# Optimization experiments

Measured on AMD Instinct MI355X. Metric: run time of the kernel, lower is better.

The kernel has to match this reference:

```python
import jax, jax.numpy as jnp
import numpy as np

H, KVH, D = 32, 8, 64  # n_heads, n_kv_heads, head_dim
NREP = H // KVH


def _rope(x, cos, sin):
    # x: (B,T,h,D); cos/sin: (T, D//2)
    half = x.shape[-1] // 2
    x1, x2 = x[..., :half], x[..., half:]
    c = cos[None, :, None, :]
    s = sin[None, :, None, :]
    return jnp.concatenate([x1 * c - x2 * s, x1 * s + x2 * c], axis=-1).astype(x.dtype)


def setup_inputs() -> dict:
    key = jax.random.key(0)
    k1, k2, k3 = jax.random.split(key, 3)
    B, T, C = 1, 2048, 2048
    x = jax.random.normal(k1, (B, T, C), dtype=jnp.float32)
    # real RoPE tables (base 10000), shape (T, D//2)
    inv_freq = 1.0 / (10000.0 ** (np.arange(0, D, 2, dtype=np.float32) / D))
    t = np.arange(T, dtype=np.float32)
    freqs = np.outer(t, inv_freq)
    cos = jnp.asarray(np.cos(freqs))
    sin = jnp.asarray(np.sin(freqs))
    Wqkv = jax.random.normal(k2, (C, H * D + 2 * KVH * D), dtype=jnp.float32) * (C ** -0.5)
    Wo = jax.random.normal(k3, (H * D, C), dtype=jnp.float32) * ((H * D) ** -0.5)
    return {"x": x, "cos": cos, "sin": sin, "Wqkv": Wqkv, "Wo": Wo}


def reference(x, cos, sin, Wqkv, Wo):
    B, T, C = x.shape
    qkv = x @ Wqkv  # (B,T, H*D + 2*KVH*D)
    q = qkv[..., : H * D].reshape(B, T, H, D)
    k = qkv[..., H * D : H * D + KVH * D].reshape(B, T, KVH, D)
    v = qkv[..., H * D + KVH * D :].reshape(B, T, KVH, D)
    # cast to bf16 as in the torch module
    q, k, v = q.astype(jnp.bfloat16), k.astype(jnp.bfloat16), v.astype(jnp.bfloat16)
    q = _rope(q, cos, sin)
    k = _rope(k, cos, sin)
    # GQA without materializing repeated KV: split q heads into (kv_head, rep)
    qg = q.reshape(B, T, KVH, NREP, D)
    scale = jnp.asarray(1.0 / np.sqrt(D), dtype=jnp.bfloat16)
    scores = jnp.einsum("bqhrd,bkhd->bhrqk", qg, k) * scale  # (B,KVH,NREP,T,T) bf16
    causal = jnp.tril(jnp.ones((T, T), dtype=bool))
    scores = jnp.where(causal[None, None, None], scores, jnp.asarray(-jnp.inf, scores.dtype))
    attn = jax.nn.softmax(scores.astype(jnp.float32), axis=-1).astype(q.dtype)
    out = jnp.einsum("bhrqk,bkhd->bqhrd", attn, v).reshape(B, T, H * D)
    return out.astype(jnp.float32) @ Wo
```

## Files before the change

### kernel.cpp

```cpp
#include <hip/hip_runtime.h>
#include <hip/hip_bf16.h>
#include <cstdint>
#include <cstddef>

#define T_SEQ 2048
#define C_DIM 2048
#define NQKV  3072
#define HQ    32
#define KVH_  8
#define D_HEAD 64

using bf16x8 = __attribute__((ext_vector_type(8))) __bf16;
using f32x4  = __attribute__((ext_vector_type(4))) float;

typedef const __attribute__((address_space(1))) void* gas_ptr;
typedef __attribute__((address_space(3))) void* las_ptr;
#define GLOAD_LDS16(g, l) __builtin_amdgcn_global_load_lds((gas_ptr)(g), (las_ptr)(l), 16, 0, 0)

static __device__ __forceinline__ unsigned short f2bf(float f) {
  union { float f; unsigned int u; } v; v.f = f;
  unsigned int u = v.u;
  unsigned int r = u + 0x7fffu + ((u >> 16) & 1u);
  return (unsigned short)(r >> 16);
}
static __device__ __forceinline__ float bf2f(unsigned short s) {
  union { unsigned int u; float f; } v; v.u = ((unsigned int)s) << 16;
  return v.f;
}
static __device__ __forceinline__ bf16x8 load8(const unsigned short* p) {
  return *reinterpret_cast<const bf16x8*>(p);
}
static __device__ __forceinline__ f32x4 mfma16(bf16x8 a, bf16x8 b, f32x4 c) {
  return __builtin_amdgcn_mfma_f32_16x16x32_bf16(a, b, c, 0, 0, 0);
}

static __device__ const unsigned char kF2QG[40] = {
    15, 15, 15, 15, 14, 14, 14, 13, 13, 13, 12, 12, 12, 11, 11,
    10, 10, 9, 9, 8, 8, 7, 7, 6, 5, 4, 3,
    14, 11, 6, 2, 13, 10, 5, 1, 12, 9, 8, 4, 0};
static __device__ const unsigned char kF2SEG[40] = {
    0, 1, 2, 3, 0, 1, 2, 0, 1, 2, 0, 1, 2, 0, 1,
    0, 1, 0, 1, 0, 1, 0, 1, 0, 0, 0, 0,
    3, 2, 1, 0, 3, 2, 1, 0, 3, 2, 2, 1, 0};
static __device__ const unsigned char kQGF[16][4] = {
    {39, 0, 0, 0}, {34, 0, 0, 0}, {30, 0, 0, 0}, {26, 0, 0, 0},
    {25, 38, 0, 0}, {24, 33, 0, 0}, {23, 29, 0, 0}, {21, 22, 0, 0},
    {19, 20, 37, 0}, {17, 18, 36, 0}, {15, 16, 32, 0}, {13, 14, 28, 0},
    {10, 11, 12, 35}, {7, 8, 9, 31}, {4, 5, 6, 27}, {0, 1, 2, 3}};

__global__ __launch_bounds__(256) void cast_x_kernel(
    const float* __restrict__ x, unsigned short* __restrict__ xh) {
  const int i = (blockIdx.x * 256 + threadIdx.x) * 8;
  const float4 a = *reinterpret_cast<const float4*>(x + i);
  const float4 b = *reinterpret_cast<const float4*>(x + i + 4);
  ushort h[8];
  h[0] = f2bf(a.x); h[1] = f2bf(a.y); h[2] = f2bf(a.z); h[3] = f2bf(a.w);
  h[4] = f2bf(b.x); h[5] = f2bf(b.y); h[6] = f2bf(b.z); h[7] = f2bf(b.w);
  *reinterpret_cast<uint4*>(xh + i) = *reinterpret_cast<const uint4*>(h);
}

__global__ __launch_bounds__(256) void transpose_cast_kernel(
    const float* __restrict__ src, unsigned short* __restrict__ dhi, int R, int C) {
  __shared__ float tile[64][65];
  const int r0 = blockIdx.y * 64, c0 = blockIdx.x * 64;
  const int tid = threadIdx.x;
  const int lr = tid >> 4, lc = (tid & 15) * 4;
  for (int i = 0; i < 4; ++i) {
    const int row = lr + i * 16;
    const float4 v = *reinterpret_cast<const float4*>(&src[(size_t)(r0 + row) * C + c0 + lc]);
    tile[row][lc + 0] = v.x; tile[row][lc + 1] = v.y;
    tile[row][lc + 2] = v.z; tile[row][lc + 3] = v.w;
  }
  __syncthreads();
  for (int i = 0; i < 4; ++i) {
    const int n = lr + i * 16;
    ushort4 h;
    h.x = f2bf(tile[lc + 0][n]); h.y = f2bf(tile[lc + 1][n]);
    h.z = f2bf(tile[lc + 2][n]); h.w = f2bf(tile[lc + 3][n]);
    *reinterpret_cast<ushort4*>(&dhi[(size_t)(c0 + n) * R + r0 + lc]) = h;
  }
}

__global__ __launch_bounds__(256, 2) void gemm1_kernel(
    const unsigned short* __restrict__ Xh, const unsigned short* __restrict__ BTh,
    const float* __restrict__ cosb, const float* __restrict__ sinb,
    unsigned short* __restrict__ qkv) {
  __shared__ unsigned short Ah[64 * 64], Bh[128 * 64];
  const int tid = threadIdx.x;
  const int orig = (int)blockIdx.y * 24 + (int)blockIdx.x;
  const int wgid = (orig & 7) * 96 + (orig >> 3);
  const int n0 = (wgid % 24) * 128, m0 = (wgid / 24) * 64;
  const int lane = tid & 63, wave = tid >> 6;
  const int wm = wave >> 1, wn = wave & 1;
  const int lrow = lane & 15, g = lane >> 4;
  const int srow8 = lane >> 3, pchunk = lane & 7;
  const int swz = lrow & 7;
  f32x4 acc[2][4] = {};
  for (int kb = 0; kb < C_DIM; kb += 64) {
    __syncthreads();
    for (int p = 0; p < 2; ++p) {
      const int row = (p * 4 + wave) * 8 + srow8;
      const int gcol = (pchunk ^ srow8) * 8;
      GLOAD_LDS16(&Xh[(size_t)(m0 + row) * C_DIM + kb + gcol],
                  &Ah[row * 64 + pchunk * 8]);
    }
    for (int p = 0; p < 4; ++p) {
      const int row = (p * 4 + wave) * 8 + srow8;
      const int gcol = (pchunk ^ srow8) * 8;
      GLOAD_LDS16(&BTh[(size_t)(n0 + row) * C_DIM + kb + gcol],
                  &Bh[row * 64 + pchunk * 8]);
    }
    __syncthreads();
    for (int kk = 0; kk < 2; ++kk) {
      bf16x8 ah[2], bh[4];
      const int cc = ((kk * 4 + g) ^ swz) * 8;
      for (int i = 0; i < 2; ++i)
        ah[i] = load8(&Ah[(wm * 32 + i * 16 + lrow) * 64 + cc]);
      for (int i = 0; i < 4; ++i)
        bh[i] = load8(&Bh[(wn * 64 + i * 16 + lrow) * 64 + cc]);
      for (int mi = 0; mi < 2; ++mi)
        for (int ni = 0; ni < 4; ++ni)
          acc[mi][ni] = mfma16(ah[mi], bh[ni], acc[mi][ni]);
    }
  }
  const int colbase = n0 + wn * 64;
  const bool isv = colbase >= (C_DIM + KVH_ * D_HEAD);
  const float qsc = (colbase < C_DIM) ? 0.18033688011112042f : 1.0f;
  for (int mi = 0; mi < 2; ++mi) {
    for (int r = 0; r < 4; ++r) {
      const int trow = m0 + wm * 32 + mi * 16 + g * 4 + r;
      if (!isv) {
        for (int ni = 0; ni < 2; ++ni) {
          const int dh = ni * 16 + lrow;
          const float c = cosb[trow * 32 + dh];
          const float s = sinb[trow * 32 + dh];
          const float a = bf2f(f2bf(acc[mi][ni][r]));
          const float b = bf2f(f2bf(acc[mi][ni + 2][r]));
          qkv[(size_t)trow * NQKV + colbase + dh]      = f2bf((a * c - b * s) * qsc);
          qkv[(size_t)trow * NQKV + colbase + dh + 32] = f2bf((a * s + b * c) * qsc);
        }
      } else {
        for (int ni = 0; ni < 4; ++ni)
          qkv[(size_t)trow * NQKV + colbase + ni * 16 + lrow] = f2bf(acc[mi][ni][r]);
      }
    }
  }
}

__global__ __launch_bounds__(256) void vt_kernel(const unsigned short* __restrict__ qkv,
                                                 unsigned short* __restrict__ vt) {
  __shared__ unsigned short tile[64][72];
  const int t0 = blockIdx.x * 64, j0 = blockIdx.y * 64;
  const int tid = threadIdx.x;
  const int lr = tid >> 4, lc = (tid & 15) * 4;
  for (int i = 0; i < 4; ++i) {
    const int row = lr + i * 16;
    const ushort4 v = *reinterpret_cast<const ushort4*>(
        &qkv[(size_t)(t0 + row) * NQKV + (C_DIM + KVH_ * D_HEAD) + j0 + lc]);
    *reinterpret_cast<ushort4*>(&tile[row][lc]) = v;
  }
  __syncthreads();
  for (int i = 0; i < 4; ++i) {
    const int j = lr + i * 16;
    ushort4 v;
    v.x = tile[lc + 0][j]; v.y = tile[lc + 1][j];
    v.z = tile[lc + 2][j]; v.w = tile[lc + 3][j];
    *reinterpret_cast<ushort4*>(&vt[(size_t)(j0 + j) * T_SEQ + t0 + lc]) = v;
  }
}

__global__ __launch_bounds__(256, 3) void attn_seg_kernel(
    const unsigned short* __restrict__ qkv, const unsigned short* __restrict__ Vt,
    unsigned short* __restrict__ po, float2* __restrict__ pml) {
  __shared__ unsigned short kbuf[2][64 * 64];
  __shared__ unsigned short vbuf[2][64 * 64];
  __shared__ unsigned short plds[4][2][16][72];
  const int f = blockIdx.x, h = blockIdx.y;
  const int qg = kF2QG[f];
  const int seg = kF2SEG[f];
  const int slot = h * 40 + f;
  const int tid = threadIdx.x;
  const int wave = tid >> 6, lane = tid & 63;
  const int kvh = h >> 2;
  const int q0b = qg * 128;
  const int q0 = q0b + wave * 32;
  const int lrow = lane & 15, g = lane >> 4;

  const int t0 = seg * 8;
  const int t1 = min(t0 + 8, 2 * qg + 2);

  const int srow = lane >> 3;
  const int schunk = (lane & 7) ^ srow;
  const unsigned short* Kg = qkv + C_DIM + kvh * D_HEAD;

  bf16x8 qf[2][2];
  for (int qs = 0; qs < 2; ++qs)
    for (int dc = 0; dc < 2; ++dc)
      qf[qs][dc] = load8(&qkv[(size_t)(q0 + qs * 16 + lrow) * NQKV + h * D_HEAD + dc * 32 + g * 8]);

  f32x4 o[2][4] = {};
  float l_[2] = {0.f, 0.f};
  const int swz = (lrow & 7);

  {
    const int k00 = t0 * 64;
    for (int j = 0; j < 2; ++j) {
      const int r0 = wave * 16 + j * 8;
      GLOAD_LDS16(Kg + (size_t)(k00 + r0 + srow) * NQKV + schunk * 8,
                  &kbuf[0][r0 * 64 + lane * 8]);
      GLOAD_LDS16(Vt + (size_t)(kvh * 64 + r0 + srow) * T_SEQ + k00 + schunk * 8,
                  &vbuf[0][r0 * 64 + lane * 8]);
    }
  }
  __syncthreads();

  for (int t = t0; t < t1; ++t) {
    const int cur = (t - t0) & 1;
    const int k0 = t * 64;
    if (t + 1 < t1) {
      const int k0n = k0 + 64;
      for (int j = 0; j < 2; ++j) {
        const int r0 = wave * 16 + j * 8;
        GLOAD_LDS16(Kg + (size_t)(k0n + r0 + srow) * NQKV + schunk * 8,
                    &kbuf[cur ^ 1][r0 * 64 + lane * 8]);
        GLOAD_LDS16(Vt + (size_t)(kvh * 64 + r0 + srow) * T_SEQ + k0n + schunk * 8,
                    &vbuf[cur ^ 1][r0 * 64 + lane * 8]);
      }
    }

    if (k0 <= q0 + 31) {
      const bool maskt = (k0 + 63 > q0);

      f32x4 s[4][2] = {};
      __builtin_amdgcn_s_setprio(1);
      for (int kt = 0; kt < 4; ++kt) {
        const unsigned short* krow = &kbuf[cur][(kt * 16 + lrow) * 64];
        const bf16x8 kf0 = load8(krow + ((0 * 4 + g) ^ swz) * 8);
        const bf16x8 kf1 = load8(krow + ((1 * 4 + g) ^ swz) * 8);
        for (int qs = 0; qs < 2; ++qs) {
          s[kt][qs] = mfma16(kf0, qf[qs][0], s[kt][qs]);
          s[kt][qs] = mfma16(kf1, qf[qs][1], s[kt][qs]);
        }
      }
      __builtin_amdgcn_s_setprio(0);

      for (int qs = 0; qs < 2; ++qs) {
        float rs = 0.f;
        for (int kt = 0; kt < 4; ++kt)
          for (int r = 0; r < 4; ++r) {
            float v = (float)(__bf16)(s[kt][qs][r]);
            if (maskt) {
              const int ka = k0 + kt * 16 + 4 * g + r;
              const int qa = q0 + qs * 16 + lrow;
              v = (ka <= qa) ? v : -INFINITY;
            }
            const float p = __builtin_amdgcn_exp2f(v);
            s[kt][qs][r] = p;
            rs += p;
          }
        l_[qs] += rs;
      }

      for (int qs = 0; qs < 2; ++qs)
        for (int kt = 0; kt < 4; ++kt) {
          union { __bf16 h4[4]; unsigned long long u; } w;
          for (int r = 0; r < 4; ++r) w.h4[r] = (__bf16)(s[kt][qs][r]);
          *reinterpret_cast<unsigned long long*>(
              &plds[wave][qs][lrow][kt * 16 + 4 * g]) = w.u;
        }
      asm volatile("s_waitcnt lgkmcnt(0)" ::: "memory");

      __builtin_amdgcn_s_setprio(1);
      for (int kc = 0; kc < 2; ++kc) {
        const bf16x8 pf0 = load8(&plds[wave][0][lrow][kc * 32 + g * 8]);
        const bf16x8 pf1 = load8(&plds[wave][1][lrow][kc * 32 + g * 8]);
        for (int dt = 0; dt < 4; ++dt) {
          const bf16x8 vf =
              load8(&vbuf[cur][(dt * 16 + lrow) * 64 + ((kc * 4 + g) ^ swz) * 8]);
          o[0][dt] = mfma16(vf, pf0, o[0][dt]);
          o[1][dt] = mfma16(vf, pf1, o[1][dt]);
        }
      }
      __builtin_amdgcn_s_setprio(0);
    }
    __syncthreads();
  }

  for (int qs = 0; qs < 2; ++qs) {
    float lv = l_[qs];
    lv += __shfl_xor(lv, 16);
    lv += __shfl_xor(lv, 32);
    l_[qs] = lv;
  }
  unsigned short* ol = &plds[wave][0][0][0];
  for (int qs = 0; qs < 2; ++qs) {
    const float inv = 1.f / l_[qs];
    for (int dt = 0; dt < 4; ++dt) {
      union { __bf16 h4[4]; unsigned long long u; } w;
      for (int r = 0; r < 4; ++r) w.h4[r] = (__bf16)(o[qs][dt][r] * inv);
      *reinterpret_cast<unsigned long long*>(
          &ol[(qs * 16 + lrow) * 72 + dt * 16 + 4 * g]) = w.u;
    }
  }
  asm volatile("s_waitcnt lgkmcnt(0)" ::: "memory");
  for (int rr = 0; rr < 4; ++rr) {
    const int row = rr * 8 + (lane >> 3);
    const int cs = (lane & 7) * 8;
    const bf16x8 v = load8(&ol[row * 72 + cs]);
    *reinterpret_cast<bf16x8*>(
        &po[(size_t)slot * 8192 + (wave * 32 + row) * 64 + cs]) = v;
  }
  if (g == 0)
    for (int qs = 0; qs < 2; ++qs)
      pml[slot * 128 + wave * 32 + qs * 16 + lrow] = make_float2(0.f, l_[qs]);
}

__global__ __launch_bounds__(256) void attn_combine_kernel(
    const unsigned short* __restrict__ po, const float2* __restrict__ pml,
    unsigned short* __restrict__ aout) {
  const int qg = blockIdx.x, h = blockIdx.y;
  const int nseg = (2 * qg + 9) / 8;
  const int tid = threadIdx.x;
  const int row = tid >> 1, c0 = (tid & 1) * 32;
  float L = 0.f, w[4];
  for (int s = 0; s < nseg; ++s) {
    const int slot = h * 40 + kQGF[qg][s];
    w[s] = pml[slot * 128 + row].y;
    L += w[s];
  }
  float acc[32] = {};
  for (int s = 0; s < nseg; ++s) {
    const int slot = h * 40 + kQGF[qg][s];
    const unsigned short* p = &po[(size_t)slot * 8192 + row * 64 + c0];
    for (int j = 0; j < 4; ++j) {
      const bf16x8 v = load8(p + j * 8);
      for (int e = 0; e < 8; ++e) acc[j * 8 + e] += w[s] * (float)v[e];
    }
  }
  const float invL = 1.f / L;
  for (int j = 0; j < 4; ++j) {
    __bf16 ov[8];
    for (int e = 0; e < 8; ++e) ov[e] = (__bf16)(acc[j * 8 + e] * invL);
    *reinterpret_cast<bf16x8*>(
        &aout[(size_t)(qg * 128 + row) * C_DIM + h * D_HEAD + c0 + j * 8]) =
        *reinterpret_cast<const bf16x8*>(ov);
  }
}

__global__ __launch_bounds__(256, 2) void gemm3_kernel(
    const unsigned short* __restrict__ A, const unsigned short* __restrict__ BT,
    float* __restrict__ out) {
  __shared__ unsigned short As[64 * 64], Bs[128 * 64];
  const int tid = threadIdx.x;
  const int orig = (int)blockIdx.y * 16 + (int)blockIdx.x;
  const int wgid = (orig & 7) * 64 + (orig >> 3);
  const int n0 = (wgid % 16) * 128, m0 = (wgid / 16) * 64;
  const int lane = tid & 63, wave = tid >> 6;
  const int wm = wave >> 1, wn = wave & 1;
  const int lrow = lane & 15, g = lane >> 4;
  const int srow8 = lane >> 3, pchunk = lane & 7;
  const int swz = lrow & 7;
  f32x4 acc[2][4] = {};
  for (int kb = 0; kb < C_DIM; kb += 64) {
    __syncthreads();
    for (int p = 0; p < 2; ++p) {
      const int row = (p * 4 + wave) * 8 + srow8;
      const int gcol = (pchunk ^ srow8) * 8;
      GLOAD_LDS16(&A[(size_t)(m0 + row) * C_DIM + kb + gcol],
                  &As[row * 64 + pchunk * 8]);
    }
    for (int p = 0; p < 4; ++p) {
      const int row = (p * 4 + wave) * 8 + srow8;
      const int gcol = (pchunk ^ srow8) * 8;
      GLOAD_LDS16(&BT[(size_t)(n0 + row) * C_DIM + kb + gcol],
                  &Bs[row * 64 + pchunk * 8]);
    }
    __syncthreads();
    for (int kk = 0; kk < 2; ++kk) {
      bf16x8 af[2], bfr[4];
      const int cc = ((kk * 4 + g) ^ swz) * 8;
      for (int i = 0; i < 2; ++i)
        af[i] = load8(&As[(wm * 32 + i * 16 + lrow) * 64 + cc]);
      for (int i = 0; i < 4; ++i)
        bfr[i] = load8(&Bs[(wn * 64 + i * 16 + lrow) * 64 + cc]);
      for (int mi = 0; mi < 2; ++mi)
        for (int ni = 0; ni < 4; ++ni)
          acc[mi][ni] = mfma16(af[mi], bfr[ni], acc[mi][ni]);
    }
  }
  for (int mi = 0; mi < 2; ++mi)
    for (int ni = 0; ni < 4; ++ni)
      for (int r = 0; r < 4; ++r)
        out[(size_t)(m0 + wm * 32 + mi * 16 + g * 4 + r) * C_DIM +
            n0 + wn * 64 + ni * 16 + lrow] = acc[mi][ni][r];
}

extern "C" void kernel_launch(void* const* d_in, const int* in_sizes, int n_in,
                              void* d_out, int out_size, void* d_ws, size_t ws_size,
                              hipStream_t stream) {
  (void)in_sizes; (void)n_in; (void)out_size; (void)ws_size;
  const float* x    = (const float*)d_in[0];
  const float* cosb = (const float*)d_in[1];
  const float* sinb = (const float*)d_in[2];
  const float* Wqkv = (const float*)d_in[3];
  const float* Wo   = (const float*)d_in[4];
  float* out = (float*)d_out;

  unsigned short* WqkvT_hi = (unsigned short*)d_ws;
  unsigned short* WoT      = WqkvT_hi + (size_t)NQKV * C_DIM;
  unsigned short* qkv      = WoT + (size_t)C_DIM * C_DIM;
  unsigned short* Vt       = qkv + (size_t)T_SEQ * NQKV;
  unsigned short* aout     = Vt + (size_t)KVH_ * D_HEAD * T_SEQ;
  unsigned short* Xh       = aout + (size_t)T_SEQ * C_DIM;
  unsigned short* po  = Xh;
  float2*         pml = (float2*)d_ws;

  cast_x_kernel<<<(T_SEQ * C_DIM) / (256 * 8), 256, 0, stream>>>(x, Xh);
  transpose_cast_kernel<<<dim3(NQKV / 64, C_DIM / 64), 256, 0, stream>>>(
      Wqkv, WqkvT_hi, C_DIM, NQKV);
  transpose_cast_kernel<<<dim3(C_DIM / 64, C_DIM / 64), 256, 0, stream>>>(
      Wo, WoT, C_DIM, C_DIM);
  gemm1_kernel<<<dim3(24, 32), 256, 0, stream>>>(Xh, WqkvT_hi, cosb, sinb, qkv);
  vt_kernel<<<dim3(T_SEQ / 64, (KVH_ * D_HEAD) / 64), 256, 0, stream>>>(qkv, Vt);
  attn_seg_kernel<<<dim3(40, HQ), 256, 0, stream>>>(qkv, Vt, po, pml);
  attn_combine_kernel<<<dim3(16, HQ), 256, 0, stream>>>(po, pml, aout);
  gemm3_kernel<<<dim3(16, 32), 256, 0, stream>>>(aout, WoT, out);
}
```

Before: 133.9 us.

## Shrink attention KV tile from 64 to 32 keys to cut LDS footprint

Halves the key/value tile held in shared memory per pipeline step (32 keys instead of 64), with a new swizzle for the narrower V tile and a smaller P staging buffer. It also stages the output epilogue per 16-row half so it fits in the reduced P buffer. The intent is to lower LDS use so more blocks can be resident and causal masking wastes less work, at the cost of twice as many loop iterations, barriers and loads per segment.

```diff
diff --git a/kernel.cpp b/kernel.cpp
--- a/kernel.cpp
+++ b/kernel.cpp
@@ -172,9 +172,9 @@
 __global__ __launch_bounds__(256, 3) void attn_seg_kernel(
     const unsigned short* __restrict__ qkv, const unsigned short* __restrict__ Vt,
     unsigned short* __restrict__ po, float2* __restrict__ pml) {
-  __shared__ unsigned short kbuf[2][64 * 64];
-  __shared__ unsigned short vbuf[2][64 * 64];
-  __shared__ unsigned short plds[4][2][16][72];
+  __shared__ unsigned short kbuf[2][32 * 64];
+  __shared__ unsigned short vbuf[2][64 * 32];
+  __shared__ unsigned short plds[4][2][16][40];
   const int f = blockIdx.x, h = blockIdx.y;
   const int qg = kF2QG[f];
   const int seg = kF2SEG[f];
@@ -182,16 +182,18 @@
   const int tid = threadIdx.x;
   const int wave = tid >> 6, lane = tid & 63;
   const int kvh = h >> 2;
-  const int q0b = qg * 128;
-  const int q0 = q0b + wave * 32;
+  const int q0 = qg * 128 + wave * 32;
   const int lrow = lane & 15, g = lane >> 4;
 
-  const int t0 = seg * 8;
-  const int t1 = min(t0 + 8, 2 * qg + 2);
-
-  const int srow = lane >> 3;
-  const int schunk = (lane & 7) ^ srow;
+  const int t0 = seg * 16;
+  const int t1 = min(t0 + 16, 4 * qg + 4);
+
+  const int ksrow = lane >> 3;
+  const int kchunk = (lane & 7) ^ ksrow;
+  const int vsrow = lane >> 2;
+  const int vchunk = (lane & 3) ^ (vsrow & 3);
   const unsigned short* Kg = qkv + C_DIM + kvh * D_HEAD;
+  const unsigned short* Vg = Vt + (size_t)(kvh * 64) * T_SEQ;
 
   bf16x8 qf[2][2];
   for (int qs = 0; qs < 2; ++qs)
@@ -201,39 +203,34 @@
   f32x4 o[2][4] = {};
   float l_[2] = {0.f, 0.f};
   const int swz = (lrow & 7);
+  const int vswz = (lrow & 3);
 
   {
-    const int k00 = t0 * 64;
-    for (int j = 0; j < 2; ++j) {
-      const int r0 = wave * 16 + j * 8;
-      GLOAD_LDS16(Kg + (size_t)(k00 + r0 + srow) * NQKV + schunk * 8,
-                  &kbuf[0][r0 * 64 + lane * 8]);
-      GLOAD_LDS16(Vt + (size_t)(kvh * 64 + r0 + srow) * T_SEQ + k00 + schunk * 8,
-                  &vbuf[0][r0 * 64 + lane * 8]);
-    }
+    const int k00 = t0 * 32;
+    GLOAD_LDS16(Kg + (size_t)(k00 + wave * 8 + ksrow) * NQKV + kchunk * 8,
+                &kbuf[0][(wave * 8) * 64 + lane * 8]);
+    GLOAD_LDS16(Vg + (size_t)(wave * 16 + vsrow) * T_SEQ + k00 + vchunk * 8,
+                &vbuf[0][(wave * 16) * 32 + lane * 8]);
   }
   __syncthreads();
 
   for (int t = t0; t < t1; ++t) {
     const int cur = (t - t0) & 1;
-    const int k0 = t * 64;
+    const int k0 = t * 32;
     if (t + 1 < t1) {
-      const int k0n = k0 + 64;
-      for (int j = 0; j < 2; ++j) {
-        const int r0 = wave * 16 + j * 8;
-        GLOAD_LDS16(Kg + (size_t)(k0n + r0 + srow) * NQKV + schunk * 8,
-                    &kbuf[cur ^ 1][r0 * 64 + lane * 8]);
-        GLOAD_LDS16(Vt + (size_t)(kvh * 64 + r0 + srow) * T_SEQ + k0n + schunk * 8,
-                    &vbuf[cur ^ 1][r0 * 64 + lane * 8]);
-      }
+      const int k0n = k0 + 32;
+      GLOAD_LDS16(Kg + (size_t)(k0n + wave * 8 + ksrow) * NQKV + kchunk * 8,
+                  &kbuf[cur ^ 1][(wave * 8) * 64 + lane * 8]);
+      GLOAD_LDS16(Vg + (size_t)(wave * 16 + vsrow) * T_SEQ + k0n + vchunk * 8,
+                  &vbuf[cur ^ 1][(wave * 16) * 32 + lane * 8]);
     }
 
     if (k0 <= q0 + 31) {
-      const bool maskt = (k0 + 63 > q0);
-
-      f32x4 s[4][2] = {};
+      const bool maskt = (k0 + 31 > q0);
+
+      f32x4 s[2][2] = {};
       __builtin_amdgcn_s_setprio(1);
-      for (int kt = 0; kt < 4; ++kt) {
+      for (int kt = 0; kt < 2; ++kt) {
         const unsigned short* krow = &kbuf[cur][(kt * 16 + lrow) * 64];
         const bf16x8 kf0 = load8(krow + ((0 * 4 + g) ^ swz) * 8);
         const bf16x8 kf1 = load8(krow + ((1 * 4 + g) ^ swz) * 8);
@@ -246,7 +243,7 @@
 
       for (int qs = 0; qs < 2; ++qs) {
         float rs = 0.f;
-        for (int kt = 0; kt < 4; ++kt)
+        for (int kt = 0; kt < 2; ++kt)
           for (int r = 0; r < 4; ++r) {
             float v = (float)(__bf16)(s[kt][qs][r]);
             if (maskt) {
@@ -262,7 +259,7 @@
       }
 
       for (int qs = 0; qs < 2; ++qs)
-        for (int kt = 0; kt < 4; ++kt) {
+        for (int kt = 0; kt < 2; ++kt) {
           union { __bf16 h4[4]; unsigned long long u; } w;
           for (int r = 0; r < 4; ++r) w.h4[r] = (__bf16)(s[kt][qs][r]);
           *reinterpret_cast<unsigned long long*>(
@@ -271,12 +268,12 @@
       asm volatile("s_waitcnt lgkmcnt(0)" ::: "memory");
 
       __builtin_amdgcn_s_setprio(1);
-      for (int kc = 0; kc < 2; ++kc) {
-        const bf16x8 pf0 = load8(&plds[wave][0][lrow][kc * 32 + g * 8]);
-        const bf16x8 pf1 = load8(&plds[wave][1][lrow][kc * 32 + g * 8]);
+      {
+        const bf16x8 pf0 = load8(&plds[wave][0][lrow][g * 8]);
+        const bf16x8 pf1 = load8(&plds[wave][1][lrow][g * 8]);
         for (int dt = 0; dt < 4; ++dt) {
           const bf16x8 vf =
-              load8(&vbuf[cur][(dt * 16 + lrow) * 64 + ((kc * 4 + g) ^ swz) * 8]);
+              load8(&vbuf[cur][(dt * 16 + lrow) * 32 + (g ^ vswz) * 8]);
           o[0][dt] = mfma16(vf, pf0, o[0][dt]);
           o[1][dt] = mfma16(vf, pf1, o[1][dt]);
         }
@@ -299,16 +296,17 @@
       union { __bf16 h4[4]; unsigned long long u; } w;
       for (int r = 0; r < 4; ++r) w.h4[r] = (__bf16)(o[qs][dt][r] * inv);
       *reinterpret_cast<unsigned long long*>(
-          &ol[(qs * 16 + lrow) * 72 + dt * 16 + 4 * g]) = w.u;
-    }
-  }
-  asm volatile("s_waitcnt lgkmcnt(0)" ::: "memory");
-  for (int rr = 0; rr < 4; ++rr) {
-    const int row = rr * 8 + (lane >> 3);
-    const int cs = (lane & 7) * 8;
-    const bf16x8 v = load8(&ol[row * 72 + cs]);
-    *reinterpret_cast<bf16x8*>(
-        &po[(size_t)slot * 8192 + (wave * 32 + row) * 64 + cs]) = v;
+          &ol[lrow * 72 + dt * 16 + 4 * g]) = w.u;
+    }
+    asm volatile("s_waitcnt lgkmcnt(0)" ::: "memory");
+    for (int rr = 0; rr < 2; ++rr) {
+      const int row = rr * 8 + (lane >> 3);
+      const int cs = (lane & 7) * 8;
+      const bf16x8 v = load8(&ol[row * 72 + cs]);
+      *reinterpret_cast<bf16x8*>(
+          &po[(size_t)slot * 8192 + (wave * 32 + qs * 16 + row) * 64 + cs]) = v;
+    }
+    asm volatile("s_waitcnt lgkmcnt(0)" ::: "memory");
   }
   if (g == 0)
     for (int qs = 0; qs < 2; ++qs)
```

After: 134.6 us. About the same (+0.6%).
